# Performance work log

Measured on AMD Instinct MI355X. Metric: run time of the kernel, lower is better.

Reference implementation:

```python
import jax, jax.numpy as jnp
import numpy as np

N_NODES = 100000
N_EDGES = 1600000
IN_FEATS, HIDDEN, N_CLASSES = 128, 64, 16


def gcn_layer(x, src, dst, W, b, n_nodes):
    # DGL GraphConv, norm='both': h = D_in^{-1/2} A (D_out^{-1/2} x) W + b
    # (W applied before aggregation since in_feats > out_feats, as DGL does)
    ones = jnp.ones((src.shape[0],), dtype=x.dtype)
    deg_out = jax.ops.segment_sum(ones, src, num_segments=n_nodes)
    deg_in = jax.ops.segment_sum(ones, dst, num_segments=n_nodes)
    norm_src = jax.lax.rsqrt(jnp.clip(deg_out, 1.0))  # [N]
    norm_dst = jax.lax.rsqrt(jnp.clip(deg_in, 1.0))   # [N]
    h = (x * norm_src[:, None]) @ W                    # [N, out]
    msgs = h[src]                                      # [E, out] gather
    agg = jax.ops.segment_sum(msgs, dst, num_segments=n_nodes)  # [N, out]
    return agg * norm_dst[:, None] + b


def setup_inputs() -> dict:
    key = jax.random.key(0)
    k1, k2, k3, k4, k5, k6, k7 = jax.random.split(key, 7)
    x = jax.random.normal(k1, (N_NODES, IN_FEATS), dtype=jnp.float32)
    src = jax.random.randint(k2, (N_EDGES,), 0, N_NODES, dtype=jnp.int32)
    dst = jax.random.randint(k3, (N_EDGES,), 0, N_NODES, dtype=jnp.int32)
    s1 = 1.0 / np.sqrt(IN_FEATS)
    s2 = 1.0 / np.sqrt(HIDDEN)
    W1 = jax.random.uniform(k4, (IN_FEATS, HIDDEN), jnp.float32, -s1, s1)
    b1 = jnp.zeros((HIDDEN,), dtype=jnp.float32)
    W2 = jax.random.uniform(k5, (HIDDEN, N_CLASSES), jnp.float32, -s2, s2)
    b2 = jnp.zeros((N_CLASSES,), dtype=jnp.float32)
    return {"x": x, "src": src, "dst": dst, "W1": W1, "b1": b1, "W2": W2, "b2": b2}


def reference(x, src, dst, W1, b1, W2, b2):
    h = gcn_layer(x, src, dst, W1, b1, N_NODES)
    h = jax.nn.relu(h)
    h = gcn_layer(h, src, dst, W2, b2, N_NODES)
    return jax.nn.softmax(h, axis=-1)  # [N, num_classes]
```

## Files before the change

### kernel.cpp

```cpp
#include <hip/hip_runtime.h>
#include <hip/hip_fp16.h>
#include <math.h>


constexpr int N_NODES = 100000;
constexpr int N_EDGES = 1600000;
constexpr int IN_F    = 128;
constexpr int HID     = 64;
constexpr int NC      = 16;

constexpr int NB_D   = 391;
constexpr int STR    = 4608;
constexpr int NBLK_P = 256;
constexpr int EPB    = N_EDGES / NBLK_P;
constexpr int CAPB   = 64;
constexpr int CSTR   = 16;

typedef _Float16 f16x8 __attribute__((ext_vector_type(8)));
typedef _Float16 f16x4 __attribute__((ext_vector_type(4)));
typedef float    f32x4 __attribute__((ext_vector_type(4)));

__global__ __launch_bounds__(512) void k_init(int* __restrict__ cursD,
                                              int* __restrict__ cursS) {
    int t = threadIdx.x;
    if (t < NB_D) {
        cursD[t * CSTR] = t * STR;
        cursS[t * CSTR] = t * STR;
    }
}

__global__ __launch_bounds__(1024) void k_part(const int* __restrict__ src,
                                               const int* __restrict__ dst,
                                               int* __restrict__ cursD,
                                               int* __restrict__ cursS,
                                               unsigned int* __restrict__ ebufD,
                                               unsigned char* __restrict__ ebufS) {
    __shared__ unsigned int  bufD[NB_D * CAPB];
    __shared__ unsigned char bufS[NB_D * CAPB];
    __shared__ int cD[NB_D], cS[NB_D], baseD[NB_D], baseS[NB_D];
    const int t = threadIdx.x, b = blockIdx.x;
    for (int i = t; i < NB_D; i += 1024) { cD[i] = 0; cS[i] = 0; }
    __syncthreads();
    const int beg = b * EPB, end = beg + EPB;
    for (int i = beg + t; i < end; i += 1024) {
        int d = dst[i], s = src[i];
        int bD = d >> 8;
        int c  = atomicAdd(&cD[bD], 1);
        if (c < CAPB) bufD[(bD << 6) + c] = ((unsigned)(d & 255) << 17) | (unsigned)s;
        int bS = s >> 8;
        int c2 = atomicAdd(&cS[bS], 1);
        if (c2 < CAPB) bufS[(bS << 6) + c2] = (unsigned char)(s & 255);
    }
    __syncthreads();
    for (int i = t; i < NB_D; i += 1024) {
        int c = min(cD[i], CAPB);
        cD[i] = c;
        baseD[i] = atomicAdd(&cursD[i * CSTR], c);
        int c2 = min(cS[i], CAPB);
        cS[i] = c2;
        baseS[i] = atomicAdd(&cursS[i * CSTR], c2);
    }
    __syncthreads();
    for (int slot = t; slot < NB_D * CAPB; slot += 1024) {
        int bk = slot >> 6, idx = slot & 63;
        if (idx < cD[bk]) ebufD[baseD[bk] + idx] = bufD[slot];
    }
    for (int slot = t; slot < NB_D * CAPB; slot += 1024) {
        int bk = slot >> 6, idx = slot & 63;
        if (idx < cS[bk]) ebufS[baseS[bk] + idx] = bufS[slot];
    }
}

__global__ __launch_bounds__(256) void k_bmerge(const int* __restrict__ cursD,
                                                const int* __restrict__ cursS,
                                                const unsigned int* __restrict__ ebufD,
                                                const unsigned char* __restrict__ ebufS,
                                                int* __restrict__ row_start,
                                                int* __restrict__ row_end,
                                                float* __restrict__ norm_dst,
                                                float* __restrict__ norm_src,
                                                int* __restrict__ csr_src) {
    __shared__ unsigned int ebl[STR];
    __shared__ int csr_l[STR];
    __shared__ int cnt[256];
    __shared__ int curs[256];
    __shared__ int wsum[4];
    const int t = threadIdx.x;
    int b = blockIdx.x;
    if (b < NB_D) {
        const int beg = b * STR;
        const int total = cursD[b * CSTR] - beg;
        for (int i = t; i < total; i += 256) ebl[i] = ebufD[beg + i];
        cnt[t] = 0;
        __syncthreads();
        for (int i = t; i < total; i += 256)
            atomicAdd(&cnt[ebl[i] >> 17], 1);
        __syncthreads();
        int x = cnt[t];
        int v = x;
        int lane = t & 63, wid = t >> 6;
        #pragma unroll
        for (int d = 1; d < 64; d <<= 1) { int u = __shfl_up(v, d, 64); if (lane >= d) v += u; }
        if (lane == 63) wsum[wid] = v;
        __syncthreads();
        int woff = 0;
        for (int w = 0; w < wid; ++w) woff += wsum[w];
        int rs = woff + v - x;
        int node = b * 256 + t;
        if (node < N_NODES) {
            row_start[node] = beg + rs;
            row_end[node]   = beg + rs + x;
            norm_dst[node]  = 1.0f / sqrtf(fmaxf((float)x, 1.0f));
        }
        curs[t] = rs;
        __syncthreads();
        for (int i = t; i < total; i += 256) {
            unsigned int e = ebl[i];
            int pos = atomicAdd(&curs[e >> 17], 1);
            csr_l[pos] = (int)(e & 0x1FFFFu);
        }
        __syncthreads();
        for (int i = t; i < total; i += 256)
            csr_src[beg + i] = csr_l[i];
    } else {
        b -= NB_D;
        const int beg = b * STR, end = cursS[b * CSTR];
        cnt[t] = 0;
        __syncthreads();
        for (int i = beg + t; i < end; i += 256)
            atomicAdd(&cnt[ebufS[i]], 1);
        __syncthreads();
        int node = b * 256 + t;
        if (node < N_NODES)
            norm_src[node] = 1.0f / sqrtf(fmaxf((float)cnt[t], 1.0f));
    }
}

constexpr int PADK = 136;
__global__ __launch_bounds__(256) void k_gemm1(
        const float* __restrict__ x, const float* __restrict__ W1,
        const float* __restrict__ norm_src, __half* __restrict__ h1h) {
    __shared__ _Float16 xh[64 * PADK];
    __shared__ _Float16 wt[64 * PADK];
    const int t = threadIdx.x;
    const int row0 = blockIdx.x * 64;
    for (int i = t; i < 64 * 32; i += 256) {
        int c4 = i & 31, rr = i >> 5;
        int gr = row0 + rr;
        float4 v = (gr < N_NODES) ? *(const float4*)&x[(size_t)gr * IN_F + c4 * 4]
                                  : float4{0.f, 0.f, 0.f, 0.f};
        f16x4 hv;
        hv[0] = (_Float16)v.x; hv[1] = (_Float16)v.y;
        hv[2] = (_Float16)v.z; hv[3] = (_Float16)v.w;
        *(f16x4*)&xh[rr * PADK + c4 * 4] = hv;
    }
    for (int i = t; i < 64 * 32; i += 256) {
        int n = i & 63, kq = i >> 6;
        int k0 = kq * 4;
        f16x4 hv;
        #pragma unroll
        for (int j = 0; j < 4; ++j)
            hv[j] = (_Float16)W1[(size_t)(k0 + j) * HID + n];
        *(f16x4*)&wt[n * PADK + k0] = hv;
    }
    __syncthreads();
    const int w = t >> 6;
    const int l = t & 63;
    const int m = l & 15, q = l >> 4;
    f32x4 acc0 = {0,0,0,0}, acc1 = {0,0,0,0}, acc2 = {0,0,0,0}, acc3 = {0,0,0,0};
    #pragma unroll
    for (int kc = 0; kc < 4; ++kc) {
        f16x8 af = *(const f16x8*)&xh[(16 * w + m) * PADK + kc * 32 + q * 8];
        f16x8 b0 = *(const f16x8*)&wt[( 0 + m) * PADK + kc * 32 + q * 8];
        f16x8 b1 = *(const f16x8*)&wt[(16 + m) * PADK + kc * 32 + q * 8];
        f16x8 b2 = *(const f16x8*)&wt[(32 + m) * PADK + kc * 32 + q * 8];
        f16x8 b3 = *(const f16x8*)&wt[(48 + m) * PADK + kc * 32 + q * 8];
        acc0 = __builtin_amdgcn_mfma_f32_16x16x32_f16(af, b0, acc0, 0, 0, 0);
        acc1 = __builtin_amdgcn_mfma_f32_16x16x32_f16(af, b1, acc1, 0, 0, 0);
        acc2 = __builtin_amdgcn_mfma_f32_16x16x32_f16(af, b2, acc2, 0, 0, 0);
        acc3 = __builtin_amdgcn_mfma_f32_16x16x32_f16(af, b3, acc3, 0, 0, 0);
    }
    _Float16* out = (_Float16*)h1h;
    #pragma unroll
    for (int r = 0; r < 4; ++r) {
        int row_g = row0 + 16 * w + q * 4 + r;
        if (row_g < N_NODES) {
            float ns = norm_src[row_g];
            size_t base = (size_t)row_g * HID + m;
            out[base +  0] = (_Float16)(acc0[r] * ns);
            out[base + 16] = (_Float16)(acc1[r] * ns);
            out[base + 32] = (_Float16)(acc2[r] * ns);
            out[base + 48] = (_Float16)(acc3[r] * ns);
        }
    }
}

__global__ __launch_bounds__(256) void k_agg1(
        const int* __restrict__ row_start, const int* __restrict__ row_end,
        const int* __restrict__ csr_src, const __half* __restrict__ h1h,
        const float* __restrict__ nd, const float* __restrict__ ns,
        const float* __restrict__ b1, const float* __restrict__ W2,
        __half* __restrict__ h2h) {
    __shared__ float W2t[16 * 68];
    __shared__ float rb[32 * 68];
    const int t = threadIdx.x;
    for (int i = t; i < HID * NC; i += 256) {
        int k = i >> 4, c = i & 15;
        W2t[c * 68 + k] = W2[i];
    }
    __syncthreads();
    const int w = t >> 6, l = t & 63;
    const int g = l >> 3, j = l & 7;
    const int nl = w * 8 + g;
    const int node = blockIdx.x * 32 + nl;
    const int beg = row_start[node], end = row_end[node];
    float a0=0,a1=0,a2=0,a3=0,a4=0,a5=0,a6=0,a7=0;
    int p = beg;
    for (; p + 8 <= end; p += 8) {
        float4 g4[8];
        #pragma unroll
        for (int u = 0; u < 8; ++u) {
            int s = csr_src[p + u];
            g4[u] = *(const float4*)&h1h[(size_t)s * HID + j * 8];
        }
        #pragma unroll
        for (int u = 0; u < 8; ++u) {
            const __half2* hh = (const __half2*)&g4[u];
            float2 f0 = __half22float2(hh[0]);
            float2 f1 = __half22float2(hh[1]);
            float2 f2 = __half22float2(hh[2]);
            float2 f3 = __half22float2(hh[3]);
            a0 += f0.x; a1 += f0.y; a2 += f1.x; a3 += f1.y;
            a4 += f2.x; a5 += f2.y; a6 += f3.x; a7 += f3.y;
        }
    }
    for (; p < end; ++p) {
        int s = csr_src[p];
        float4 g4 = *(const float4*)&h1h[(size_t)s * HID + j * 8];
        const __half2* hh = (const __half2*)&g4;
        float2 f0 = __half22float2(hh[0]);
        float2 f1 = __half22float2(hh[1]);
        float2 f2 = __half22float2(hh[2]);
        float2 f3 = __half22float2(hh[3]);
        a0 += f0.x; a1 += f0.y; a2 += f1.x; a3 += f1.y;
        a4 += f2.x; a5 += f2.y; a6 += f3.x; a7 += f3.y;
    }
    const float n = nd[node];
    const float4 bb0 = *(const float4*)&b1[j * 8 + 0];
    const float4 bb1 = *(const float4*)&b1[j * 8 + 4];
    float4 v0, v1;
    v0.x = fmaxf(a0 * n + bb0.x, 0.f);
    v0.y = fmaxf(a1 * n + bb0.y, 0.f);
    v0.z = fmaxf(a2 * n + bb0.z, 0.f);
    v0.w = fmaxf(a3 * n + bb0.w, 0.f);
    v1.x = fmaxf(a4 * n + bb1.x, 0.f);
    v1.y = fmaxf(a5 * n + bb1.y, 0.f);
    v1.z = fmaxf(a6 * n + bb1.z, 0.f);
    v1.w = fmaxf(a7 * n + bb1.w, 0.f);
    *(float4*)&rb[nl * 68 + j * 8 + 0] = v0;
    *(float4*)&rb[nl * 68 + j * 8 + 4] = v1;
    float o0 = 0.f, o1 = 0.f;
    #pragma unroll
    for (int k4 = 0; k4 < 16; ++k4) {
        float4 r  = *(float4*)&rb[nl * 68 + k4 * 4];
        float4 wa = *(float4*)&W2t[j * 68 + k4 * 4];
        float4 wb = *(float4*)&W2t[(j + 8) * 68 + k4 * 4];
        o0 += r.x * wa.x + r.y * wa.y + r.z * wa.z + r.w * wa.w;
        o1 += r.x * wb.x + r.y * wb.y + r.z * wb.z + r.w * wb.w;
    }
    const float nsv = ns[node];
    _Float16* o = (_Float16*)h2h;
    o[(size_t)node * NC + j]     = (_Float16)(o0 * nsv);
    o[(size_t)node * NC + j + 8] = (_Float16)(o1 * nsv);
}

__global__ __launch_bounds__(256) void k_agg2(
        const int* __restrict__ row_start, const int* __restrict__ row_end,
        const int* __restrict__ csr_src, const __half* __restrict__ h2h,
        const float* __restrict__ nd, const float* __restrict__ b2,
        float* __restrict__ out) {
    int t = threadIdx.x;
    int node = blockIdx.x * 128 + (t >> 1);
    int sub = t & 1;
    if (node >= N_NODES) return;
    int beg = row_start[node], end = row_end[node];
    float acc[8] = {0,0,0,0,0,0,0,0};
    int p = beg;
    for (; p + 8 <= end; p += 8) {
        float4 g[8];
        #pragma unroll
        for (int u = 0; u < 8; ++u) {
            int s = csr_src[p + u];
            g[u] = *(const float4*)&h2h[(size_t)s * NC + sub * 8];
        }
        #pragma unroll
        for (int u = 0; u < 8; ++u) {
            const __half2* hh = (const __half2*)&g[u];
            #pragma unroll
            for (int j = 0; j < 4; ++j) {
                float2 f = __half22float2(hh[j]);
                acc[j * 2 + 0] += f.x; acc[j * 2 + 1] += f.y;
            }
        }
    }
    for (; p < end; ++p) {
        int s = csr_src[p];
        float4 g = *(const float4*)&h2h[(size_t)s * NC + sub * 8];
        const __half2* hh = (const __half2*)&g;
        #pragma unroll
        for (int j = 0; j < 4; ++j) {
            float2 f = __half22float2(hh[j]);
            acc[j * 2 + 0] += f.x; acc[j * 2 + 1] += f.y;
        }
    }
    float n = nd[node];
    float v[8];
    #pragma unroll
    for (int j = 0; j < 8; ++j) v[j] = acc[j] * n + b2[sub * 8 + j];
    float m = v[0];
    #pragma unroll
    for (int j = 1; j < 8; ++j) m = fmaxf(m, v[j]);
    m = fmaxf(m, __shfl_xor(m, 1, 2));
    float e[8]; float s = 0.f;
    #pragma unroll
    for (int j = 0; j < 8; ++j) { e[j] = __expf(v[j] - m); s += e[j]; }
    s += __shfl_xor(s, 1, 2);
    float inv = 1.0f / s;
    float4 o0 = { e[0]*inv, e[1]*inv, e[2]*inv, e[3]*inv };
    float4 o1 = { e[4]*inv, e[5]*inv, e[6]*inv, e[7]*inv };
    *(float4*)&out[(size_t)node * NC + sub * 8 + 0] = o0;
    *(float4*)&out[(size_t)node * NC + sub * 8 + 4] = o1;
}

extern "C" void kernel_launch(void* const* d_in, const int* in_sizes, int n_in,
                              void* d_out, int out_size, void* d_ws, size_t ws_size,
                              hipStream_t stream) {
    const float* x   = (const float*)d_in[0];
    const int*   src = (const int*)  d_in[1];
    const int*   dst = (const int*)  d_in[2];
    const float* W1  = (const float*)d_in[3];
    const float* b1  = (const float*)d_in[4];
    const float* W2  = (const float*)d_in[5];
    const float* b2  = (const float*)d_in[6];
    float* out = (float*)d_out;

    const size_t N = N_NODES;
    float* ws       = (float*)d_ws;
    int*   wsI      = (int*)d_ws;
    float* norm_src = ws;
    float* norm_dst = ws + N;
    __half* h1h     = (__half*)(ws + 2 * N);
    __half* h2h     = (__half*)(ws + 34 * N);
    unsigned int*  ebufD = (unsigned int*)(wsI + 66 * N);
    unsigned char* ebufS = (unsigned char*)(wsI + 66 * N + NB_D * STR);
    int*   row_st   = wsI + 130 * N;
    int*   row_en   = wsI + 131 * N;
    int*   cursD    = wsI + 132 * N;
    int*   cursS    = wsI + 132 * N + 8192;
    int*   csr_src  = wsI + 132 * N + 16384;

    k_init<<<1, 512, 0, stream>>>(cursD, cursS);
    k_part<<<NBLK_P, 1024, 0, stream>>>(src, dst, cursD, cursS, ebufD, ebufS);
    k_bmerge<<<2 * NB_D, 256, 0, stream>>>(cursD, cursS, ebufD, ebufS,
                                           row_st, row_en, norm_dst, norm_src,
                                           csr_src);
    k_gemm1<<<(N_NODES + 63) / 64, 256, 0, stream>>>(x, W1, norm_src, h1h);
    k_agg1<<<N_NODES / 32, 256, 0, stream>>>(row_st, row_en, csr_src, h1h,
                                             norm_dst, norm_src, b1, W2, h2h);
    k_agg2<<<(N_NODES + 127) / 128, 256, 0, stream>>>(row_st, row_en, csr_src, h2h,
                                                      norm_dst, b2, out);
}
```

Before: 201.2 us.

## Fuse per-bucket CSR build into aggregation kernels, dropping global CSR arrays

```diff
diff --git a/kernel.cpp b/kernel.cpp
--- a/kernel.cpp
+++ b/kernel.cpp
@@ -71,69 +71,22 @@
     }
 }
 
-__global__ __launch_bounds__(256) void k_bmerge(const int* __restrict__ cursD,
-                                                const int* __restrict__ cursS,
-                                                const unsigned int* __restrict__ ebufD,
-                                                const unsigned char* __restrict__ ebufS,
-                                                int* __restrict__ row_start,
-                                                int* __restrict__ row_end,
-                                                float* __restrict__ norm_dst,
-                                                float* __restrict__ norm_src,
-                                                int* __restrict__ csr_src) {
-    __shared__ unsigned int ebl[STR];
-    __shared__ int csr_l[STR];
+__global__ __launch_bounds__(256) void k_bmergeS(const int* __restrict__ cursS,
+                                                 const unsigned char* __restrict__ ebufS,
+                                                 float* __restrict__ norm_src) {
     __shared__ int cnt[256];
-    __shared__ int curs[256];
-    __shared__ int wsum[4];
-    const int t = threadIdx.x;
-    int b = blockIdx.x;
-    if (b < NB_D) {
-        const int beg = b * STR;
-        const int total = cursD[b * CSTR] - beg;
-        for (int i = t; i < total; i += 256) ebl[i] = ebufD[beg + i];
-        cnt[t] = 0;
-        __syncthreads();
-        for (int i = t; i < total; i += 256)
-            atomicAdd(&cnt[ebl[i] >> 17], 1);
-        __syncthreads();
-        int x = cnt[t];
-        int v = x;
-        int lane = t & 63, wid = t >> 6;
-        #pragma unroll
-        for (int d = 1; d < 64; d <<= 1) { int u = __shfl_up(v, d, 64); if (lane >= d) v += u; }
-        if (lane == 63) wsum[wid] = v;
-        __syncthreads();
-        int woff = 0;
-        for (int w = 0; w < wid; ++w) woff += wsum[w];
-        int rs = woff + v - x;
-        int node = b * 256 + t;
-        if (node < N_NODES) {
-            row_start[node] = beg + rs;
-            row_end[node]   = beg + rs + x;
-            norm_dst[node]  = 1.0f / sqrtf(fmaxf((float)x, 1.0f));
-        }
-        curs[t] = rs;
-        __syncthreads();
-        for (int i = t; i < total; i += 256) {
-            unsigned int e = ebl[i];
-            int pos = atomicAdd(&curs[e >> 17], 1);
-            csr_l[pos] = (int)(e & 0x1FFFFu);
-        }
-        __syncthreads();
-        for (int i = t; i < total; i += 256)
-            csr_src[beg + i] = csr_l[i];
-    } else {
-        b -= NB_D;
-        const int beg = b * STR, end = cursS[b * CSTR];
-        cnt[t] = 0;
-        __syncthreads();
-        for (int i = beg + t; i < end; i += 256)
-            atomicAdd(&cnt[ebufS[i]], 1);
-        __syncthreads();
-        int node = b * 256 + t;
-        if (node < N_NODES)
-            norm_src[node] = 1.0f / sqrtf(fmaxf((float)cnt[t], 1.0f));
-    }
+    const int t = threadIdx.x, b = blockIdx.x;
+    const int beg = b * STR;
+    int end = cursS[b * CSTR];
+    if (end > beg + STR) end = beg + STR;
+    cnt[t] = 0;
+    __syncthreads();
+    for (int i = beg + t; i < end; i += 256)
+        atomicAdd(&cnt[ebufS[i]], 1);
+    __syncthreads();
+    int node = b * 256 + t;
+    if (node < N_NODES)
+        norm_src[node] = 1.0f / sqrtf(fmaxf((float)cnt[t], 1.0f));
 }
 
 constexpr int PADK = 136;
@@ -195,37 +148,88 @@
     }
 }
 
-__global__ __launch_bounds__(256) void k_agg1(
-        const int* __restrict__ row_start, const int* __restrict__ row_end,
-        const int* __restrict__ csr_src, const __half* __restrict__ h1h,
-        const float* __restrict__ nd, const float* __restrict__ ns,
+__global__ __launch_bounds__(1024) void k_agg1(
+        const int* __restrict__ cursD, const unsigned int* __restrict__ ebufD,
+        const __half* __restrict__ h1h, const float* __restrict__ ns,
         const float* __restrict__ b1, const float* __restrict__ W2,
         __half* __restrict__ h2h) {
+    __shared__ unsigned int ebl[STR];
+    __shared__ int csr_l[STR];
+    __shared__ float rb[128 * 68];
     __shared__ float W2t[16 * 68];
-    __shared__ float rb[32 * 68];
-    const int t = threadIdx.x;
-    for (int i = t; i < HID * NC; i += 256) {
+    __shared__ int cnt[256], curs[256], rs_l[256], wsum[4];
+    const int t = threadIdx.x, b = blockIdx.x;
+    const int beg = b * STR;
+    int total = cursD[b * CSTR] - beg;
+    if (total > STR) total = STR;
+    const int nv = total >> 2;
+    const uint4* s4 = (const uint4*)(ebufD + beg);
+    for (int i = t; i < nv; i += 1024) ((uint4*)ebl)[i] = s4[i];
+    for (int i = (nv << 2) + t; i < total; i += 1024) ebl[i] = ebufD[beg + i];
+    if (t < 256) cnt[t] = 0;
+    for (int i = t; i < HID * NC; i += 1024) {
         int k = i >> 4, c = i & 15;
         W2t[c * 68 + k] = W2[i];
     }
     __syncthreads();
-    const int w = t >> 6, l = t & 63;
-    const int g = l >> 3, j = l & 7;
-    const int nl = w * 8 + g;
-    const int node = blockIdx.x * 32 + nl;
-    const int beg = row_start[node], end = row_end[node];
-    float a0=0,a1=0,a2=0,a3=0,a4=0,a5=0,a6=0,a7=0;
-    int p = beg;
-    for (; p + 8 <= end; p += 8) {
-        float4 g4[8];
-        #pragma unroll
-        for (int u = 0; u < 8; ++u) {
-            int s = csr_src[p + u];
-            g4[u] = *(const float4*)&h1h[(size_t)s * HID + j * 8];
-        }
-        #pragma unroll
-        for (int u = 0; u < 8; ++u) {
-            const __half2* hh = (const __half2*)&g4[u];
+    for (int i = t; i < total; i += 1024)
+        atomicAdd(&cnt[ebl[i] >> 17], 1);
+    __syncthreads();
+    int x = 0, v = 0;
+    const int lane = t & 63, wid = t >> 6;
+    if (t < 256) {
+        x = cnt[t]; v = x;
+        #pragma unroll
+        for (int d = 1; d < 64; d <<= 1) { int u = __shfl_up(v, d, 64); if (lane >= d) v += u; }
+        if (lane == 63) wsum[wid] = v;
+    }
+    __syncthreads();
+    if (t < 256) {
+        int woff = 0;
+        for (int ww = 0; ww < wid; ++ww) woff += wsum[ww];
+        int rs = woff + v - x;
+        rs_l[t] = rs;
+        curs[t] = rs;
+    }
+    __syncthreads();
+    for (int i = t; i < total; i += 1024) {
+        unsigned int e = ebl[i];
+        int pos = atomicAdd(&curs[e >> 17], 1);
+        csr_l[pos] = (int)(e & 0x1FFFFu);
+    }
+    __syncthreads();
+    const int w = t >> 6, l = t & 63, g = l >> 3, j = l & 7;
+    const float4 bb0 = *(const float4*)&b1[j * 8 + 0];
+    const float4 bb1 = *(const float4*)&b1[j * 8 + 4];
+    #pragma unroll
+    for (int pp = 0; pp < 2; ++pp) {
+        const int nl = pp * 128 + w * 8 + g;
+        const int pbeg = rs_l[nl], deg = cnt[nl];
+        const int pend = pbeg + deg;
+        float a0=0,a1=0,a2=0,a3=0,a4=0,a5=0,a6=0,a7=0;
+        int p = pbeg;
+        for (; p + 8 <= pend; p += 8) {
+            float4 g4[8];
+            #pragma unroll
+            for (int u = 0; u < 8; ++u) {
+                int s = csr_l[p + u];
+                g4[u] = *(const float4*)&h1h[(size_t)s * HID + j * 8];
+            }
+            #pragma unroll
+            for (int u = 0; u < 8; ++u) {
+                const __half2* hh = (const __half2*)&g4[u];
+                float2 f0 = __half22float2(hh[0]);
+                float2 f1 = __half22float2(hh[1]);
+                float2 f2 = __half22float2(hh[2]);
+                float2 f3 = __half22float2(hh[3]);
+                a0 += f0.x; a1 += f0.y; a2 += f1.x; a3 += f1.y;
+                a4 += f2.x; a5 += f2.y; a6 += f3.x; a7 += f3.y;
+            }
+        }
+        for (; p < pend; ++p) {
+            int s = csr_l[p];
+            float4 g4 = *(const float4*)&h1h[(size_t)s * HID + j * 8];
+            const __half2* hh = (const __half2*)&g4;
             float2 f0 = __half22float2(hh[0]);
             float2 f1 = __half22float2(hh[1]);
             float2 f2 = __half22float2(hh[2]);
@@ -233,103 +237,131 @@
             a0 += f0.x; a1 += f0.y; a2 += f1.x; a3 += f1.y;
             a4 += f2.x; a5 += f2.y; a6 += f3.x; a7 += f3.y;
         }
-    }
-    for (; p < end; ++p) {
-        int s = csr_src[p];
-        float4 g4 = *(const float4*)&h1h[(size_t)s * HID + j * 8];
-        const __half2* hh = (const __half2*)&g4;
+        const float n = 1.0f / sqrtf(fmaxf((float)deg, 1.0f));
+        float4 v0, v1;
+        v0.x = fmaxf(a0 * n + bb0.x, 0.f);
+        v0.y = fmaxf(a1 * n + bb0.y, 0.f);
+        v0.z = fmaxf(a2 * n + bb0.z, 0.f);
+        v0.w = fmaxf(a3 * n + bb0.w, 0.f);
+        v1.x = fmaxf(a4 * n + bb1.x, 0.f);
+        v1.y = fmaxf(a5 * n + bb1.y, 0.f);
+        v1.z = fmaxf(a6 * n + bb1.z, 0.f);
+        v1.w = fmaxf(a7 * n + bb1.w, 0.f);
+        const int rrow = w * 8 + g;
+        *(float4*)&rb[rrow * 68 + j * 8 + 0] = v0;
+        *(float4*)&rb[rrow * 68 + j * 8 + 4] = v1;
+        float o0 = 0.f, o1 = 0.f;
+        #pragma unroll
+        for (int k4 = 0; k4 < 16; ++k4) {
+            float4 r  = *(float4*)&rb[rrow * 68 + k4 * 4];
+            float4 wa = *(float4*)&W2t[j * 68 + k4 * 4];
+            float4 wb = *(float4*)&W2t[(j + 8) * 68 + k4 * 4];
+            o0 += r.x * wa.x + r.y * wa.y + r.z * wa.z + r.w * wa.w;
+            o1 += r.x * wb.x + r.y * wb.y + r.z * wb.z + r.w * wb.w;
+        }
+        const int node = b * 256 + nl;
+        if (node < N_NODES) {
+            const float nsv = ns[node];
+            _Float16* o = (_Float16*)h2h;
+            o[(size_t)node * NC + j]     = (_Float16)(o0 * nsv);
+            o[(size_t)node * NC + j + 8] = (_Float16)(o1 * nsv);
+        }
+    }
+}
+
+__global__ __launch_bounds__(1024) void k_agg2(
+        const int* __restrict__ cursD, const unsigned int* __restrict__ ebufD,
+        const __half* __restrict__ h2h, const float* __restrict__ b2,
+        float* __restrict__ out) {
+    __shared__ unsigned int ebl[STR];
+    __shared__ int csr_l[STR];
+    __shared__ int cnt[256], curs[256], rs_l[256], wsum[4];
+    const int t = threadIdx.x, b = blockIdx.x;
+    const int beg = b * STR;
+    int total = cursD[b * CSTR] - beg;
+    if (total > STR) total = STR;
+    const int nv = total >> 2;
+    const uint4* s4 = (const uint4*)(ebufD + beg);
+    for (int i = t; i < nv; i += 1024) ((uint4*)ebl)[i] = s4[i];
+    for (int i = (nv << 2) + t; i < total; i += 1024) ebl[i] = ebufD[beg + i];
+    if (t < 256) cnt[t] = 0;
+    __syncthreads();
+    for (int i = t; i < total; i += 1024)
+        atomicAdd(&cnt[ebl[i] >> 17], 1);
+    __syncthreads();
+    int x = 0, v = 0;
+    const int lane = t & 63, wid = t >> 6;
+    if (t < 256) {
+        x = cnt[t]; v = x;
+        #pragma unroll
+        for (int d = 1; d < 64; d <<= 1) { int u = __shfl_up(v, d, 64); if (lane >= d) v += u; }
+        if (lane == 63) wsum[wid] = v;
+    }
+    __syncthreads();
+    if (t < 256) {
+        int woff = 0;
+        for (int ww = 0; ww < wid; ++ww) woff += wsum[ww];
+        int rs = woff + v - x;
+        rs_l[t] = rs;
+        curs[t] = rs;
+    }
+    __syncthreads();
+    for (int i = t; i < total; i += 1024) {
+        unsigned int e = ebl[i];
+        int pos = atomicAdd(&curs[e >> 17], 1);
+        csr_l[pos] = (int)(e & 0x1FFFFu);
+    }
+    __syncthreads();
+    const int w = t >> 6, l = t & 63, g = l >> 2, sub = l & 3;
+    const int nl = w * 16 + g;
+    const int pbeg = rs_l[nl], deg = cnt[nl];
+    const int pend = pbeg + deg;
+    float acc[4] = {0, 0, 0, 0};
+    int p = pbeg;
+    for (; p + 8 <= pend; p += 8) {
+        float2 g8[8];
+        #pragma unroll
+        for (int u = 0; u < 8; ++u) {
+            int s = csr_l[p + u];
+            g8[u] = *(const float2*)&h2h[(size_t)s * NC + sub * 4];
+        }
+        #pragma unroll
+        for (int u = 0; u < 8; ++u) {
+            const __half2* hh = (const __half2*)&g8[u];
+            float2 f0 = __half22float2(hh[0]);
+            float2 f1 = __half22float2(hh[1]);
+            acc[0] += f0.x; acc[1] += f0.y; acc[2] += f1.x; acc[3] += f1.y;
+        }
+    }
+    for (; p < pend; ++p) {
+        int s = csr_l[p];
+        float2 g2 = *(const float2*)&h2h[(size_t)s * NC + sub * 4];
+        const __half2* hh = (const __half2*)&g2;
         float2 f0 = __half22float2(hh[0]);
         float2 f1 = __half22float2(hh[1]);
-        float2 f2 = __half22float2(hh[2]);
-        float2 f3 = __half22float2(hh[3]);
-        a0 += f0.x; a1 += f0.y; a2 += f1.x; a3 += f1.y;
-        a4 += f2.x; a5 += f2.y; a6 += f3.x; a7 += f3.y;
-    }
-    const float n = nd[node];
-    const float4 bb0 = *(const float4*)&b1[j * 8 + 0];
-    const float4 bb1 = *(const float4*)&b1[j * 8 + 4];
-    float4 v0, v1;
-    v0.x = fmaxf(a0 * n + bb0.x, 0.f);
-    v0.y = fmaxf(a1 * n + bb0.y, 0.f);
-    v0.z = fmaxf(a2 * n + bb0.z, 0.f);
-    v0.w = fmaxf(a3 * n + bb0.w, 0.f);
-    v1.x = fmaxf(a4 * n + bb1.x, 0.f);
-    v1.y = fmaxf(a5 * n + bb1.y, 0.f);
-    v1.z = fmaxf(a6 * n + bb1.z, 0.f);
-    v1.w = fmaxf(a7 * n + bb1.w, 0.f);
-    *(float4*)&rb[nl * 68 + j * 8 + 0] = v0;
-    *(float4*)&rb[nl * 68 + j * 8 + 4] = v1;
-    float o0 = 0.f, o1 = 0.f;
-    #pragma unroll
-    for (int k4 = 0; k4 < 16; ++k4) {
-        float4 r  = *(float4*)&rb[nl * 68 + k4 * 4];
-        float4 wa = *(float4*)&W2t[j * 68 + k4 * 4];
-        float4 wb = *(float4*)&W2t[(j + 8) * 68 + k4 * 4];
-        o0 += r.x * wa.x + r.y * wa.y + r.z * wa.z + r.w * wa.w;
-        o1 += r.x * wb.x + r.y * wb.y + r.z * wb.z + r.w * wb.w;
-    }
-    const float nsv = ns[node];
-    _Float16* o = (_Float16*)h2h;
-    o[(size_t)node * NC + j]     = (_Float16)(o0 * nsv);
-    o[(size_t)node * NC + j + 8] = (_Float16)(o1 * nsv);
-}
-
-__global__ __launch_bounds__(256) void k_agg2(
-        const int* __restrict__ row_start, const int* __restrict__ row_end,
-        const int* __restrict__ csr_src, const __half* __restrict__ h2h,
-        const float* __restrict__ nd, const float* __restrict__ b2,
-        float* __restrict__ out) {
-    int t = threadIdx.x;
-    int node = blockIdx.x * 128 + (t >> 1);
-    int sub = t & 1;
-    if (node >= N_NODES) return;
-    int beg = row_start[node], end = row_end[node];
-    float acc[8] = {0,0,0,0,0,0,0,0};
-    int p = beg;
-    for (; p + 8 <= end; p += 8) {
-        float4 g[8];
-        #pragma unroll
-        for (int u = 0; u < 8; ++u) {
-            int s = csr_src[p + u];
-            g[u] = *(const float4*)&h2h[(size_t)s * NC + sub * 8];
-        }
-        #pragma unroll
-        for (int u = 0; u < 8; ++u) {
-            const __half2* hh = (const __half2*)&g[u];
-            #pragma unroll
-            for (int j = 0; j < 4; ++j) {
-                float2 f = __half22float2(hh[j]);
-                acc[j * 2 + 0] += f.x; acc[j * 2 + 1] += f.y;
-            }
-        }
-    }
-    for (; p < end; ++p) {
-        int s = csr_src[p];
-        float4 g = *(const float4*)&h2h[(size_t)s * NC + sub * 8];
-        const __half2* hh = (const __half2*)&g;
-        #pragma unroll
-        for (int j = 0; j < 4; ++j) {
-            float2 f = __half22float2(hh[j]);
-            acc[j * 2 + 0] += f.x; acc[j * 2 + 1] += f.y;
-        }
-    }
-    float n = nd[node];
-    float v[8];
-    #pragma unroll
-    for (int j = 0; j < 8; ++j) v[j] = acc[j] * n + b2[sub * 8 + j];
-    float m = v[0];
-    #pragma unroll
-    for (int j = 1; j < 8; ++j) m = fmaxf(m, v[j]);
-    m = fmaxf(m, __shfl_xor(m, 1, 2));
-    float e[8]; float s = 0.f;
-    #pragma unroll
-    for (int j = 0; j < 8; ++j) { e[j] = __expf(v[j] - m); s += e[j]; }
-    s += __shfl_xor(s, 1, 2);
-    float inv = 1.0f / s;
-    float4 o0 = { e[0]*inv, e[1]*inv, e[2]*inv, e[3]*inv };
-    float4 o1 = { e[4]*inv, e[5]*inv, e[6]*inv, e[7]*inv };
-    *(float4*)&out[(size_t)node * NC + sub * 8 + 0] = o0;
-    *(float4*)&out[(size_t)node * NC + sub * 8 + 4] = o1;
+        acc[0] += f0.x; acc[1] += f0.y; acc[2] += f1.x; acc[3] += f1.y;
+    }
+    const float n = 1.0f / sqrtf(fmaxf((float)deg, 1.0f));
+    const float4 bv = *(const float4*)&b2[sub * 4];
+    float vv[4];
+    vv[0] = acc[0] * n + bv.x;
+    vv[1] = acc[1] * n + bv.y;
+    vv[2] = acc[2] * n + bv.z;
+    vv[3] = acc[3] * n + bv.w;
+    float m = fmaxf(fmaxf(vv[0], vv[1]), fmaxf(vv[2], vv[3]));
+    m = fmaxf(m, __shfl_xor(m, 1, 4));
+    m = fmaxf(m, __shfl_xor(m, 2, 4));
+    float e0 = __expf(vv[0] - m), e1 = __expf(vv[1] - m);
+    float e2 = __expf(vv[2] - m), e3 = __expf(vv[3] - m);
+    float s = e0 + e1 + e2 + e3;
+    s += __shfl_xor(s, 1, 4);
+    s += __shfl_xor(s, 2, 4);
+    const float inv = 1.0f / s;
+    const int node = b * 256 + nl;
+    if (node < N_NODES) {
+        float4 o4 = { e0 * inv, e1 * inv, e2 * inv, e3 * inv };
+        *(float4*)&out[(size_t)node * NC + sub * 4] = o4;
+    }
 }
 
 extern "C" void kernel_launch(void* const* d_in, const int* in_sizes, int n_in,
@@ -348,25 +380,17 @@
     float* ws       = (float*)d_ws;
     int*   wsI      = (int*)d_ws;
     float* norm_src = ws;
-    float* norm_dst = ws + N;
     __half* h1h     = (__half*)(ws + 2 * N);
     __half* h2h     = (__half*)(ws + 34 * N);
     unsigned int*  ebufD = (unsigned int*)(wsI + 66 * N);
     unsigned char* ebufS = (unsigned char*)(wsI + 66 * N + NB_D * STR);
-    int*   row_st   = wsI + 130 * N;
-    int*   row_en   = wsI + 131 * N;
     int*   cursD    = wsI + 132 * N;
     int*   cursS    = wsI + 132 * N + 8192;
-    int*   csr_src  = wsI + 132 * N + 16384;
 
     k_init<<<1, 512, 0, stream>>>(cursD, cursS);
     k_part<<<NBLK_P, 1024, 0, stream>>>(src, dst, cursD, cursS, ebufD, ebufS);
-    k_bmerge<<<2 * NB_D, 256, 0, stream>>>(cursD, cursS, ebufD, ebufS,
-                                           row_st, row_en, norm_dst, norm_src,
-                                           csr_src);
+    k_bmergeS<<<NB_D, 256, 0, stream>>>(cursS, ebufS, norm_src);
     k_gemm1<<<(N_NODES + 63) / 64, 256, 0, stream>>>(x, W1, norm_src, h1h);
-    k_agg1<<<N_NODES / 32, 256, 0, stream>>>(row_st, row_en, csr_src, h1h,
-                                             norm_dst, norm_src, b1, W2, h2h);
-    k_agg2<<<(N_NODES + 127) / 128, 256, 0, stream>>>(row_st, row_en, csr_src, h2h,
-                                                      norm_dst, b2, out);
-}
+    k_agg1<<<NB_D, 1024, 0, stream>>>(cursD, ebufD, h1h, norm_src, b1, W2, h2h);
+    k_agg2<<<NB_D, 1024, 0, stream>>>(cursD, ebufD, h2h, b2, out);
+}
```

Measured after the change: 198.5 us. No clear change (-1.3%).
